# Kernel tuning notes

Measured on AMD Instinct MI355X. Metric: run time of the kernel, lower is better.

The kernel has to match this reference:

```python
import jax, jax.numpy as jnp
import numpy as np
import math

B, S, D = 2, 2048, 2048
H = 16
HD = D // H          # 128
WINDOW = 256


def setup_inputs() -> dict:
    key = jax.random.key(0)
    ks = jax.random.split(key, 5)
    x = jax.random.normal(ks[0], (B, S, D), dtype=jnp.float32)
    # standard RoPE frequency tables: shape (S, HD//2)
    inv_freq = 1.0 / (10000.0 ** (np.arange(0, HD, 2, dtype=np.float32) / HD))
    t = np.arange(S, dtype=np.float32)
    ang = np.outer(t, inv_freq)  # [S, HD//2]
    freqs_cos = jnp.asarray(np.cos(ang), dtype=jnp.float32)
    freqs_sin = jnp.asarray(np.sin(ang), dtype=jnp.float32)
    scale = 0.02
    wq = jax.random.normal(ks[1], (D, D), dtype=jnp.float32) * scale
    wk = jax.random.normal(ks[2], (D, D), dtype=jnp.float32) * scale
    wv = jax.random.normal(ks[3], (D, D), dtype=jnp.float32) * scale
    wo = jax.random.normal(ks[4], (D, D), dtype=jnp.float32) * scale
    return {"x": x, "freqs_cos": freqs_cos, "freqs_sin": freqs_sin,
            "wq": wq, "wk": wk, "wv": wv, "wo": wo}


def _rope(t, cos, sin):
    # t: [B, S, H, HD]; cos/sin: [S, HD//2]
    tr = t.reshape(t.shape[:-1] + (HD // 2, 2))
    r, i = tr[..., 0], tr[..., 1]
    c = cos[None, :, None, :]
    s = sin[None, :, None, :]
    out_r = r * c - i * s
    out_i = r * s + i * c
    return jnp.stack([out_r, out_i], axis=-1).reshape(t.shape)


def _sliding_window_mask(seqlen, window):
    i = jnp.arange(seqlen)[:, None]
    j = jnp.arange(seqlen)[None, :]
    valid = (j <= i) & (j > i - window)
    return jnp.where(valid, 0.0, -jnp.inf).astype(jnp.float32)  # [S, S]


def reference(x, freqs_cos, freqs_sin, wq, wk, wv, wo):
    bsz, seqlen, _ = x.shape
    # QKV projections (nn.Linear, no bias: y = x @ W^T)
    xq = (x @ wq.T).reshape(bsz, seqlen, H, HD)
    xk = (x @ wk.T).reshape(bsz, seqlen, H, HD)
    xv = (x @ wv.T).reshape(bsz, seqlen, H, HD)
    # RoPE on q and k
    xq = _rope(xq, freqs_cos, freqs_sin)
    xk = _rope(xk, freqs_cos, freqs_sin)
    # [B, H, S, HD]
    q = xq.transpose(0, 2, 1, 3)
    k = xk.transpose(0, 2, 1, 3)
    v = xv.transpose(0, 2, 1, 3)
    mask = _sliding_window_mask(seqlen, WINDOW)  # [S, S]
    scores = jnp.einsum('bhqd,bhkd->bhqk', q, k) / math.sqrt(HD)
    scores = scores + mask[None, None, :, :]
    probs = jax.nn.softmax(scores, axis=-1)
    out = jnp.einsum('bhqk,bhkd->bhqd', probs, v)
    out = out.transpose(0, 2, 1, 3).reshape(bsz, seqlen, H * HD)
    return out @ wo.T
```

## Files before the change

kernel.cpp:

```cpp
#include <hip/hip_runtime.h>

typedef __attribute__((ext_vector_type(8))) short bf16x8;
typedef __attribute__((ext_vector_type(4))) float f32x4;

#define LOG2E 1.4426950408889634f
#define SWZ(L) ((L) ^ ((((L) >> 7) & 7) << 4))

__device__ __forceinline__ unsigned short f2bf(float f) {
  unsigned int x = __builtin_bit_cast(unsigned int, f);
  x += 0x7fffu + ((x >> 16) & 1u);
  return (unsigned short)(x >> 16);
}
__device__ __forceinline__ float bf2f(unsigned short u) {
  unsigned int x = ((unsigned int)u) << 16;
  return __builtin_bit_cast(float, x);
}

__device__ __forceinline__ void gload16(const void* g, void* l) {
  __builtin_amdgcn_global_load_lds((const __attribute__((address_space(1))) void*)g,
                                   (__attribute__((address_space(3))) void*)l, 16, 0, 0);
}

__device__ __forceinline__ bf16x8 ldsf(const char* region, int row, int colbyte) {
  const int L = row * 128 + colbyte;
  return *(const bf16x8*)(region + SWZ(L));
}

__device__ __forceinline__ void stage_half(const unsigned short* __restrict__ G, int rowbase,
                                           int K, int ku, char* region, int w, int l) {
#pragma unroll
  for (int i = 0; i < 2; ++i) {
    const int off = w * 1024 + i * 8192;
    const int P = off + l * 16;
    const int L = SWZ(P);
    const int r = L >> 7, cs = (L & 127) >> 1;
    gload16(G + (long long)(rowbase + r) * K + ku + cs, region + off);
  }
}

__global__ __launch_bounds__(256)
void cast_pack(const float* __restrict__ x, const float* __restrict__ wq,
               const float* __restrict__ wk, const float* __restrict__ wv,
               const float* __restrict__ wo,
               unsigned short* __restrict__ xb, unsigned short* __restrict__ wqkv,
               unsigned short* __restrict__ wob) {
  const int NX = 8388608, DD = 4194304;
  const int i = (blockIdx.x * 256 + threadIdx.x) * 4;
  const float* src; unsigned short* dst; float scale = 1.0f;
  if (i < NX)               { src = x + i;                    dst = xb + i; }
  else if (i < NX + DD)     { int o = i - NX;      src = wq + o; dst = wqkv + o; scale = 0.088388347648318447f; }
  else if (i < NX + 2*DD)   { int o = i - NX - DD;   src = wk + o; dst = wqkv + DD + o; }
  else if (i < NX + 3*DD)   { int o = i - NX - 2*DD; src = wv + o; dst = wqkv + 2*DD + o; }
  else                      { int o = i - NX - 3*DD; src = wo + o; dst = wob + o; }
  const float4 v = *(const float4*)src;
  ushort4 u;
  u.x = f2bf(v.x * scale); u.y = f2bf(v.y * scale);
  u.z = f2bf(v.z * scale); u.w = f2bf(v.w * scale);
  *(ushort4*)dst = u;
}

template<int MODE>
__global__ __launch_bounds__(512, 2)
void gemm256(const unsigned short* __restrict__ A, const unsigned short* __restrict__ Bw,
             float* __restrict__ Of, unsigned short* __restrict__ Qb,
             unsigned short* __restrict__ Kb, unsigned short* __restrict__ Vt,
             const float* __restrict__ fc, const float* __restrict__ fs, int K) {
  __shared__ char lds[98304];
  char* const Abase = lds;
  char* const Bbase = lds + 32768;
  const int tid = threadIdx.x;
  const int l = tid & 63, w = tid >> 6;
  const int wr = w >> 2, wc = w & 3;
  const int lq = l & 15, g = l >> 4;
  const int nwg = gridDim.x;
  const int cpx = nwg >> 3;
  const int orig = blockIdx.x;
  const int wg = (orig & 7) * cpx + (orig >> 3);
  const int bm = wg & 31, bn = wg >> 5;
  const unsigned short* Ab = A + (long long)bm * 128 * K;
  const unsigned short* Bb = Bw + (long long)bn * 256 * K;
  const int NT = K >> 6;

  stage_half(Bb, 0,   K, 0,  Bbase,         w, l);
  stage_half(Bb, 128, K, 0,  Bbase + 16384, w, l);
  stage_half(Ab, 0,   K, 0,  Abase,         w, l);
  stage_half(Bb, 0,   K, 64, Bbase + 32768, w, l);
  stage_half(Bb, 128, K, 64, Bbase + 49152, w, l);
  asm volatile("s_waitcnt vmcnt(4)" ::: "memory");
  __builtin_amdgcn_s_barrier();

  f32x4 acc[4][4] = {};
  const int brow0 = (wc & 1) * 64;
  const int arow0 = wr * 64;
  for (int t = 0; t < NT; ++t) {
    const int d = t & 1;
    const char* Ar = Abase + d * 16384;
    const char* Br = Bbase + d * 32768 + (wc >> 1) * 16384;
    bf16x8 a0, a1, b[2][4];
#pragma unroll
    for (int kk = 0; kk < 2; ++kk)
#pragma unroll
      for (int ni = 0; ni < 4; ++ni)
        b[kk][ni] = ldsf(Br, brow0 + ni * 16 + lq, kk * 64 + g * 16);
    a0 = ldsf(Ar, arow0 + 0 * 16 + lq, g * 16);
    a1 = ldsf(Ar, arow0 + 1 * 16 + lq, g * 16);
    { const int u = t + 1; const int ku = (u < NT) ? u * 64 : 0;
      stage_half(Ab, 0, K, ku, Abase + (u & 1) * 16384, w, l); }
    asm volatile("s_waitcnt lgkmcnt(0)" ::: "memory");
    __builtin_amdgcn_sched_barrier(0);
    __builtin_amdgcn_s_setprio(1);
#pragma unroll
    for (int ni = 0; ni < 4; ++ni) {
      acc[0][ni] = __builtin_amdgcn_mfma_f32_16x16x32_bf16(a0, b[0][ni], acc[0][ni], 0, 0, 0);
      acc[1][ni] = __builtin_amdgcn_mfma_f32_16x16x32_bf16(a1, b[0][ni], acc[1][ni], 0, 0, 0);
    }
    __builtin_amdgcn_s_setprio(0);
    __builtin_amdgcn_s_barrier();
    a0 = ldsf(Ar, arow0 + 2 * 16 + lq, g * 16);
    a1 = ldsf(Ar, arow0 + 3 * 16 + lq, g * 16);
    { const int u = t + 2; const int ku = (u < NT) ? u * 64 : 0;
      stage_half(Bb, 0, K, ku, Bbase + d * 32768, w, l); }
    asm volatile("s_waitcnt lgkmcnt(0)" ::: "memory");
    __builtin_amdgcn_sched_barrier(0);
    __builtin_amdgcn_s_setprio(1);
#pragma unroll
    for (int ni = 0; ni < 4; ++ni) {
      acc[2][ni] = __builtin_amdgcn_mfma_f32_16x16x32_bf16(a0, b[0][ni], acc[2][ni], 0, 0, 0);
      acc[3][ni] = __builtin_amdgcn_mfma_f32_16x16x32_bf16(a1, b[0][ni], acc[3][ni], 0, 0, 0);
    }
    __builtin_amdgcn_s_setprio(0);
    __builtin_amdgcn_s_barrier();
    a0 = ldsf(Ar, arow0 + 0 * 16 + lq, 64 + g * 16);
    a1 = ldsf(Ar, arow0 + 1 * 16 + lq, 64 + g * 16);
    { const int u = t + 2; const int ku = (u < NT) ? u * 64 : 0;
      stage_half(Bb, 128, K, ku, Bbase + d * 32768 + 16384, w, l); }
    asm volatile("s_waitcnt lgkmcnt(0)" ::: "memory");
    __builtin_amdgcn_sched_barrier(0);
    __builtin_amdgcn_s_setprio(1);
#pragma unroll
    for (int ni = 0; ni < 4; ++ni) {
      acc[0][ni] = __builtin_amdgcn_mfma_f32_16x16x32_bf16(a0, b[1][ni], acc[0][ni], 0, 0, 0);
      acc[1][ni] = __builtin_amdgcn_mfma_f32_16x16x32_bf16(a1, b[1][ni], acc[1][ni], 0, 0, 0);
    }
    __builtin_amdgcn_s_setprio(0);
    __builtin_amdgcn_s_barrier();
    a0 = ldsf(Ar, arow0 + 2 * 16 + lq, 64 + g * 16);
    a1 = ldsf(Ar, arow0 + 3 * 16 + lq, 64 + g * 16);
    asm volatile("s_waitcnt lgkmcnt(0)" ::: "memory");
    __builtin_amdgcn_sched_barrier(0);
    __builtin_amdgcn_s_setprio(1);
#pragma unroll
    for (int ni = 0; ni < 4; ++ni) {
      acc[2][ni] = __builtin_amdgcn_mfma_f32_16x16x32_bf16(a0, b[1][ni], acc[2][ni], 0, 0, 0);
      acc[3][ni] = __builtin_amdgcn_mfma_f32_16x16x32_bf16(a1, b[1][ni], acc[3][ni], 0, 0, 0);
    }
    __builtin_amdgcn_s_setprio(0);
    asm volatile("s_waitcnt vmcnt(4)" ::: "memory");
    __builtin_amdgcn_s_barrier();
  }
  asm volatile("s_waitcnt vmcnt(0)" ::: "memory");

  if (MODE == 0) {
    const int colb = bn * 256;
    if (colb < 4096) {
      unsigned short* dst = (colb < 2048) ? Qb : Kb;
      const int cb = colb & 2047;
#pragma unroll
      for (int mi = 0; mi < 4; ++mi) {
        const int row = bm * 128 + wr * 64 + mi * 16 + g * 4;
        const int s0 = row & 2047;
#pragma unroll
        for (int ni = 0; ni < 4; ++ni) {
          const int col = cb + wc * 64 + ni * 16 + lq;
          const int hd = col & 127;
          const int j = hd >> 1;
          const bool odd = hd & 1;
#pragma unroll
          for (int r = 0; r < 4; ++r) {
            const int s = s0 + r;
            const float c  = fc[s * 64 + j];
            const float sn = fs[s * 64 + j];
            const float own = acc[mi][ni][r];
            const float oth = __shfl_xor(own, 1);
            const float val = odd ? (oth * sn + own * c) : (own * c - oth * sn);
            dst[(long long)(row + r) * 2048 + col] = f2bf(val);
          }
        }
      }
    } else {
#pragma unroll
      for (int mi = 0; mi < 4; ++mi) {
        const int row = bm * 128 + wr * 64 + mi * 16 + g * 4;
        const int b = row >> 11, s = row & 2047;
#pragma unroll
        for (int ni = 0; ni < 4; ++ni) {
          const int c = colb - 4096 + wc * 64 + ni * 16 + lq;
          const int h = c >> 7, dd = c & 127;
          ushort4 o4;
          o4.x = f2bf(acc[mi][ni][0]); o4.y = f2bf(acc[mi][ni][1]);
          o4.z = f2bf(acc[mi][ni][2]); o4.w = f2bf(acc[mi][ni][3]);
          *(ushort4*)&Vt[((long long)((b * 16 + h) * 128 + dd)) * 2048 + s] = o4;
        }
      }
    }
  } else {
#pragma unroll
    for (int mi = 0; mi < 4; ++mi) {
      const int row = bm * 128 + wr * 64 + mi * 16 + g * 4;
#pragma unroll
      for (int ni = 0; ni < 4; ++ni) {
        const int col = bn * 256 + wc * 64 + ni * 16 + lq;
#pragma unroll
        for (int r = 0; r < 4; ++r)
          Of[(long long)(row + r) * 2048 + col] = acc[mi][ni][r];
      }
    }
  }
}

__global__ __launch_bounds__(256)
void attn_k(const unsigned short* __restrict__ Qb, const unsigned short* __restrict__ Kb,
            const unsigned short* __restrict__ Vt, unsigned short* __restrict__ Ob) {
  __shared__ unsigned short plds[4096];
  const int tid = threadIdx.x;
  const int l = tid & 63, w = tid >> 6;
  const int lq = l & 15, g = l >> 4;
  const int qb = blockIdx.x, bh = blockIdx.y;
  const int b = bh >> 4, h = bh & 15;
  const int q_abs = qb * 64 + w * 16 + lq;
  const unsigned short* Qrow = Qb + ((long long)(b * 2048 + q_abs)) * 2048 + h * 128;
  bf16x8 qf[4];
#pragma unroll
  for (int ks = 0; ks < 4; ++ks)
    qf[ks] = *(const bf16x8*)&Qrow[ks * 32 + g * 8];
  f32x4 o[8] = {};
  float m = -1e30f, lsum = 0.0f;
  char* pb = (char*)(plds + w * 1024);
  const unsigned short* Kbase = Kb + ((long long)(b * 2048)) * 2048 + h * 128;
  const unsigned short* Vbase = Vt + ((long long)bh) * 128 * 2048;
  const int kb_lo = (qb >= 4) ? qb - 4 : 0;
  for (int kb = kb_lo; kb <= qb; ++kb) {
    const int key0 = kb * 64;
    f32x4 sc[4] = {};
    __builtin_amdgcn_s_setprio(1);
#pragma unroll
    for (int mt = 0; mt < 4; ++mt) {
      const unsigned short* Krow = Kbase + (long long)(key0 + mt * 16 + lq) * 2048;
#pragma unroll
      for (int ks = 0; ks < 4; ++ks) {
        const bf16x8 kf = *(const bf16x8*)&Krow[ks * 32 + g * 8];
        sc[mt] = __builtin_amdgcn_mfma_f32_16x16x32_bf16(kf, qf[ks], sc[mt], 0, 0, 0);
      }
    }
    __builtin_amdgcn_s_setprio(0);
    float sv[16];
    float bmax = -1e30f;
#pragma unroll
    for (int mt = 0; mt < 4; ++mt)
#pragma unroll
      for (int r = 0; r < 4; ++r) {
        const int key = key0 + mt * 16 + g * 4 + r;
        float xv = sc[mt][r];
        const bool valid = (key <= q_abs) && (key + 256 > q_abs);
        xv = valid ? xv : -1e30f;
        sv[mt * 4 + r] = xv;
        bmax = fmaxf(bmax, xv);
      }
    bmax = fmaxf(bmax, __shfl_xor(bmax, 16));
    bmax = fmaxf(bmax, __shfl_xor(bmax, 32));
    const float mnew = fmaxf(m, bmax);
    const float rf = __builtin_exp2f((m - mnew) * LOG2E);
    float psum = 0.0f;
#pragma unroll
    for (int i = 0; i < 16; ++i) {
      const float p = __builtin_exp2f((sv[i] - mnew) * LOG2E);
      sv[i] = p;
      psum += p;
    }
    psum += __shfl_xor(psum, 16);
    psum += __shfl_xor(psum, 32);
    lsum = lsum * rf + psum;
    m = mnew;
#pragma unroll
    for (int dt = 0; dt < 8; ++dt) o[dt] *= rf;
#pragma unroll
    for (int mt = 0; mt < 4; ++mt) {
      const unsigned int lo = (unsigned int)f2bf(sv[mt * 4 + 0]) | ((unsigned int)f2bf(sv[mt * 4 + 1]) << 16);
      const unsigned int hi = (unsigned int)f2bf(sv[mt * 4 + 2]) | ((unsigned int)f2bf(sv[mt * 4 + 3]) << 16);
      int byte = lq * 128 + (mt * 16 + g * 4) * 2;
      byte ^= (lq & 7) << 4;
      *(uint2*)(pb + byte) = make_uint2(lo, hi);
    }
    asm volatile("s_waitcnt lgkmcnt(0)" ::: "memory");
    __builtin_amdgcn_sched_barrier(0);
    bf16x8 pf[2];
#pragma unroll
    for (int k2 = 0; k2 < 2; ++k2) {
      int byte = lq * 128 + k2 * 64 + g * 16;
      byte ^= (lq & 7) << 4;
      pf[k2] = *(const bf16x8*)(pb + byte);
    }
    asm volatile("s_waitcnt lgkmcnt(0)" ::: "memory");
    __builtin_amdgcn_sched_barrier(0);
    __builtin_amdgcn_s_setprio(1);
#pragma unroll
    for (int dt = 0; dt < 8; ++dt) {
      const unsigned short* Vrow = Vbase + (long long)(dt * 16 + lq) * 2048 + key0;
#pragma unroll
      for (int k2 = 0; k2 < 2; ++k2) {
        const bf16x8 vf = *(const bf16x8*)&Vrow[k2 * 32 + g * 8];
        o[dt] = __builtin_amdgcn_mfma_f32_16x16x32_bf16(vf, pf[k2], o[dt], 0, 0, 0);
      }
    }
    __builtin_amdgcn_s_setprio(0);
  }
  const float inv = 1.0f / lsum;
  unsigned short* Or = Ob + ((long long)(b * 2048 + q_abs)) * 2048 + h * 128;
#pragma unroll
  for (int dt = 0; dt < 8; ++dt) {
    ushort4 o4;
    o4.x = f2bf(o[dt][0] * inv);
    o4.y = f2bf(o[dt][1] * inv);
    o4.z = f2bf(o[dt][2] * inv);
    o4.w = f2bf(o[dt][3] * inv);
    *(ushort4*)&Or[dt * 16 + g * 4] = o4;
  }
}

extern "C" void kernel_launch(void* const* d_in, const int* in_sizes, int n_in,
                              void* d_out, int out_size, void* d_ws, size_t ws_size,
                              hipStream_t stream) {
  const float* x  = (const float*)d_in[0];
  const float* fc = (const float*)d_in[1];
  const float* fs = (const float*)d_in[2];
  const float* wq = (const float*)d_in[3];
  const float* wk = (const float*)d_in[4];
  const float* wv = (const float*)d_in[5];
  const float* wo = (const float*)d_in[6];

  unsigned short* ws   = (unsigned short*)d_ws;
  unsigned short* xb   = ws;
  unsigned short* wqkv = xb + 8388608;
  unsigned short* wob  = wqkv + 12582912;
  unsigned short* Qb   = wob + 4194304;
  unsigned short* Kb   = Qb + 8388608;
  unsigned short* Vt   = Kb + 8388608;
  unsigned short* Ob   = Vt + 8388608;

  cast_pack<<<24576, 256, 0, stream>>>(x, wq, wk, wv, wo, xb, wqkv, wob);
  gemm256<0><<<768, 512, 0, stream>>>(xb, wqkv, nullptr, Qb, Kb, Vt, fc, fs, 2048);
  attn_k<<<dim3(32, 32), 256, 0, stream>>>(Qb, Kb, Vt, Ob);
  gemm256<1><<<256, 512, 0, stream>>>(Ob, wob, (float*)d_out, nullptr, nullptr, nullptr, fc, fs, 2048);
}
```

Before: 263.1 us.

## Process two key blocks per online-softmax step in sliding-window attention

The attention loop now handles two 64-key blocks per iteration, computing both score tiles before a single max/rescale step and then running PV MFMAs over both blocks. It also skips rescaling the output accumulators when the running max does not increase. This halves the number of softmax reductions, rescales and LDS barriers per query tile and gives more independent MFMA work between synchronisation points. In exchange it doubles the LDS scratch, raises register pressure and adds branches for odd block counts.

```diff
diff --git a/kernel.cpp b/kernel.cpp
--- a/kernel.cpp
+++ b/kernel.cpp
@@ -221,7 +221,7 @@
 __global__ __launch_bounds__(256)
 void attn_k(const unsigned short* __restrict__ Qb, const unsigned short* __restrict__ Kb,
             const unsigned short* __restrict__ Vt, unsigned short* __restrict__ Ob) {
-  __shared__ unsigned short plds[4096];
+  __shared__ unsigned short plds[8192];
   const int tid = threadIdx.x;
   const int l = tid & 63, w = tid >> 6;
   const int lq = l & 15, g = l >> 4;
@@ -235,70 +235,116 @@
     qf[ks] = *(const bf16x8*)&Qrow[ks * 32 + g * 8];
   f32x4 o[8] = {};
   float m = -1e30f, lsum = 0.0f;
-  char* pb = (char*)(plds + w * 1024);
+  char* pb = (char*)(plds + w * 2048);
   const unsigned short* Kbase = Kb + ((long long)(b * 2048)) * 2048 + h * 128;
   const unsigned short* Vbase = Vt + ((long long)bh) * 128 * 2048;
   const int kb_lo = (qb >= 4) ? qb - 4 : 0;
-  for (int kb = kb_lo; kb <= qb; ++kb) {
+  for (int kb = kb_lo; kb <= qb; kb += 2) {
+    const bool hb = (kb + 1 <= qb);
     const int key0 = kb * 64;
-    f32x4 sc[4] = {};
-    __builtin_amdgcn_s_setprio(1);
-#pragma unroll
-    for (int mt = 0; mt < 4; ++mt) {
-      const unsigned short* Krow = Kbase + (long long)(key0 + mt * 16 + lq) * 2048;
-#pragma unroll
-      for (int ks = 0; ks < 4; ++ks) {
-        const bf16x8 kf = *(const bf16x8*)&Krow[ks * 32 + g * 8];
-        sc[mt] = __builtin_amdgcn_mfma_f32_16x16x32_bf16(kf, qf[ks], sc[mt], 0, 0, 0);
-      }
-    }
-    __builtin_amdgcn_s_setprio(0);
-    float sv[16];
+    float sva[16], svb[16];
+    {
+      f32x4 sc[4] = {};
+      __builtin_amdgcn_s_setprio(1);
+#pragma unroll
+      for (int mt = 0; mt < 4; ++mt) {
+        const unsigned short* Krow = Kbase + (long long)(key0 + mt * 16 + lq) * 2048;
+#pragma unroll
+        for (int ks = 0; ks < 4; ++ks) {
+          const bf16x8 kf = *(const bf16x8*)&Krow[ks * 32 + g * 8];
+          sc[mt] = __builtin_amdgcn_mfma_f32_16x16x32_bf16(kf, qf[ks], sc[mt], 0, 0, 0);
+        }
+      }
+      __builtin_amdgcn_s_setprio(0);
+#pragma unroll
+      for (int mt = 0; mt < 4; ++mt)
+#pragma unroll
+        for (int r = 0; r < 4; ++r) {
+          const int key = key0 + mt * 16 + g * 4 + r;
+          const bool valid = (key <= q_abs) && (key + 256 > q_abs);
+          sva[mt * 4 + r] = valid ? sc[mt][r] : -1e30f;
+        }
+    }
+    if (hb) {
+      f32x4 sc[4] = {};
+      __builtin_amdgcn_s_setprio(1);
+#pragma unroll
+      for (int mt = 0; mt < 4; ++mt) {
+        const unsigned short* Krow = Kbase + (long long)(key0 + 64 + mt * 16 + lq) * 2048;
+#pragma unroll
+        for (int ks = 0; ks < 4; ++ks) {
+          const bf16x8 kf = *(const bf16x8*)&Krow[ks * 32 + g * 8];
+          sc[mt] = __builtin_amdgcn_mfma_f32_16x16x32_bf16(kf, qf[ks], sc[mt], 0, 0, 0);
+        }
+      }
+      __builtin_amdgcn_s_setprio(0);
+#pragma unroll
+      for (int mt = 0; mt < 4; ++mt)
+#pragma unroll
+        for (int r = 0; r < 4; ++r) {
+          const int key = key0 + 64 + mt * 16 + g * 4 + r;
+          const bool valid = (key <= q_abs) && (key + 256 > q_abs);
+          svb[mt * 4 + r] = valid ? sc[mt][r] : -1e30f;
+        }
+    } else {
+#pragma unroll
+      for (int i = 0; i < 16; ++i) svb[i] = -1e30f;
+    }
     float bmax = -1e30f;
 #pragma unroll
-    for (int mt = 0; mt < 4; ++mt)
-#pragma unroll
-      for (int r = 0; r < 4; ++r) {
-        const int key = key0 + mt * 16 + g * 4 + r;
-        float xv = sc[mt][r];
-        const bool valid = (key <= q_abs) && (key + 256 > q_abs);
-        xv = valid ? xv : -1e30f;
-        sv[mt * 4 + r] = xv;
-        bmax = fmaxf(bmax, xv);
-      }
+    for (int i = 0; i < 16; ++i) bmax = fmaxf(bmax, fmaxf(sva[i], svb[i]));
     bmax = fmaxf(bmax, __shfl_xor(bmax, 16));
     bmax = fmaxf(bmax, __shfl_xor(bmax, 32));
     const float mnew = fmaxf(m, bmax);
-    const float rf = __builtin_exp2f((m - mnew) * LOG2E);
     float psum = 0.0f;
 #pragma unroll
     for (int i = 0; i < 16; ++i) {
-      const float p = __builtin_exp2f((sv[i] - mnew) * LOG2E);
-      sv[i] = p;
-      psum += p;
+      const float p = __builtin_exp2f((sva[i] - mnew) * LOG2E);
+      sva[i] = p; psum += p;
+    }
+#pragma unroll
+    for (int i = 0; i < 16; ++i) {
+      const float p = __builtin_exp2f((svb[i] - mnew) * LOG2E);
+      svb[i] = p; psum += p;
     }
     psum += __shfl_xor(psum, 16);
     psum += __shfl_xor(psum, 32);
-    lsum = lsum * rf + psum;
-    m = mnew;
-#pragma unroll
-    for (int dt = 0; dt < 8; ++dt) o[dt] *= rf;
+    if (mnew > m) {
+      const float rf = __builtin_exp2f((m - mnew) * LOG2E);
+      lsum = lsum * rf + psum;
+      m = mnew;
+#pragma unroll
+      for (int dt = 0; dt < 8; ++dt) o[dt] *= rf;
+    } else {
+      lsum += psum;
+    }
 #pragma unroll
     for (int mt = 0; mt < 4; ++mt) {
-      const unsigned int lo = (unsigned int)f2bf(sv[mt * 4 + 0]) | ((unsigned int)f2bf(sv[mt * 4 + 1]) << 16);
-      const unsigned int hi = (unsigned int)f2bf(sv[mt * 4 + 2]) | ((unsigned int)f2bf(sv[mt * 4 + 3]) << 16);
+      const unsigned int lo = (unsigned int)f2bf(sva[mt * 4 + 0]) | ((unsigned int)f2bf(sva[mt * 4 + 1]) << 16);
+      const unsigned int hi = (unsigned int)f2bf(sva[mt * 4 + 2]) | ((unsigned int)f2bf(sva[mt * 4 + 3]) << 16);
       int byte = lq * 128 + (mt * 16 + g * 4) * 2;
       byte ^= (lq & 7) << 4;
       *(uint2*)(pb + byte) = make_uint2(lo, hi);
     }
-    asm volatile("s_waitcnt lgkmcnt(0)" ::: "memory");
-    __builtin_amdgcn_sched_barrier(0);
-    bf16x8 pf[2];
+    if (hb) {
+#pragma unroll
+      for (int mt = 0; mt < 4; ++mt) {
+        const unsigned int lo = (unsigned int)f2bf(svb[mt * 4 + 0]) | ((unsigned int)f2bf(svb[mt * 4 + 1]) << 16);
+        const unsigned int hi = (unsigned int)f2bf(svb[mt * 4 + 2]) | ((unsigned int)f2bf(svb[mt * 4 + 3]) << 16);
+        int byte = lq * 128 + (mt * 16 + g * 4) * 2;
+        byte ^= (lq & 7) << 4;
+        *(uint2*)(pb + 2048 + byte) = make_uint2(lo, hi);
+      }
+    }
+    asm volatile("s_waitcnt lgkmcnt(0)" ::: "memory");
+    __builtin_amdgcn_sched_barrier(0);
+    bf16x8 pfa[2], pfb[2];
 #pragma unroll
     for (int k2 = 0; k2 < 2; ++k2) {
       int byte = lq * 128 + k2 * 64 + g * 16;
       byte ^= (lq & 7) << 4;
-      pf[k2] = *(const bf16x8*)(pb + byte);
+      pfa[k2] = *(const bf16x8*)(pb + byte);
+      if (hb) pfb[k2] = *(const bf16x8*)(pb + 2048 + byte);
     }
     asm volatile("s_waitcnt lgkmcnt(0)" ::: "memory");
     __builtin_amdgcn_sched_barrier(0);
@@ -309,7 +355,14 @@
 #pragma unroll
       for (int k2 = 0; k2 < 2; ++k2) {
         const bf16x8 vf = *(const bf16x8*)&Vrow[k2 * 32 + g * 8];
-        o[dt] = __builtin_amdgcn_mfma_f32_16x16x32_bf16(vf, pf[k2], o[dt], 0, 0, 0);
+        o[dt] = __builtin_amdgcn_mfma_f32_16x16x32_bf16(vf, pfa[k2], o[dt], 0, 0, 0);
+      }
+      if (hb) {
+#pragma unroll
+        for (int k2 = 0; k2 < 2; ++k2) {
+          const bf16x8 vf = *(const bf16x8*)&Vrow[64 + k2 * 32 + g * 8];
+          o[dt] = __builtin_amdgcn_mfma_f32_16x16x32_bf16(vf, pfb[k2], o[dt], 0, 0, 0);
+        }
       }
     }
     __builtin_amdgcn_s_setprio(0);
```

Result: faster. 257.8 us (-2.0%).
